# Kernel tuning notes

Measured on AMD Instinct MI355X. Metric: run time of the kernel, lower is better.

## Reference

```python
import jax, jax.numpy as jnp
import numpy as np

B, K = 4, 128
V_IN, V_OUT = 256, 256
E_IN, E_OUT = 512, 512
P_PE, T_PE = 200, 100
HEADS = 16  # c_atten_head


def _lin(key, din, dout):
    kw, kb = jax.random.split(key)
    W = jax.random.normal(kw, (din, dout), jnp.float32) / np.sqrt(din).astype(np.float32)
    b = jax.random.normal(kb, (dout,), jnp.float32) * 0.01
    return W, b


def setup_inputs() -> dict:
    key = jax.random.key(0)
    ks = jax.random.split(key, 14)
    v_f = jax.random.normal(ks[0], (B, K, V_IN), jnp.float32)
    e_f = jax.random.normal(ks[1], (B, K * K, E_IN), jnp.float32)
    p_pe = jax.random.normal(ks[2], (B, K, P_PE), jnp.float32)
    t_pe = jax.random.normal(ks[3], (B, T_PE), jnp.float32)
    e_agg_mask = (jax.random.uniform(ks[4], (B, K, K)) > 0.1).astype(jnp.float32)
    v_agg_mask = (jax.random.uniform(ks[5], (B, K)) > 0.1).astype(jnp.float32)
    W_vpe, b_vpe = _lin(ks[6], V_IN + P_PE + T_PE, V_IN)
    W_epe, b_epe = _lin(ks[7], E_IN + T_PE, E_IN)
    W_ev1, b_ev1 = _lin(ks[8], E_IN + 2 * V_IN, E_OUT)
    W_ev2, b_ev2 = _lin(ks[9], E_OUT, E_OUT)
    W_q, b_q = _lin(ks[10], V_IN, E_OUT)
    W_k, b_k = _lin(ks[11], V_IN, E_OUT)
    W_self, b_self = _lin(ks[12], V_IN, E_OUT)
    W_out, b_out = _lin(ks[13], 2 * E_OUT, V_OUT)
    return dict(v_f=v_f, e_f=e_f, p_pe=p_pe, t_pe=t_pe,
                e_agg_mask=e_agg_mask, v_agg_mask=v_agg_mask,
                W_vpe=W_vpe, b_vpe=b_vpe, W_epe=W_epe, b_epe=b_epe,
                W_ev1=W_ev1, b_ev1=b_ev1, W_ev2=W_ev2, b_ev2=b_ev2,
                W_q=W_q, b_q=b_q, W_k=W_k, b_k=b_k,
                W_self=W_self, b_self=b_self, W_out=W_out, b_out=b_out)


def reference(v_f, e_f, p_pe, t_pe, e_agg_mask, v_agg_mask,
              W_vpe, b_vpe, W_epe, b_epe, W_ev1, b_ev1, W_ev2, b_ev2,
              W_q, b_q, W_k, b_k, W_self, b_self, W_out, b_out):
    silu = jax.nn.silu
    # PE binding
    t_v = jnp.broadcast_to(t_pe[:, None, :], (B, K, T_PE))
    v = silu(jnp.concatenate([v_f, p_pe, t_v], -1) @ W_vpe + b_vpe)          # (B,K,V_IN)
    t_e = jnp.broadcast_to(t_pe[:, None, :], (B, K * K, T_PE))
    e = silu(jnp.concatenate([e_f, t_e], -1) @ W_epe + b_epe)                # (B,K*K,E_IN)
    # dense all-pairs node features -> edge values
    pair = jnp.concatenate([jnp.broadcast_to(v[:, :, None, :], (B, K, K, V_IN)),
                            jnp.broadcast_to(v[:, None, :, :], (B, K, K, V_IN))], -1)
    ev_in = jnp.concatenate([pair.reshape(B, K * K, 2 * V_IN), e], -1)
    e_value = silu(ev_in @ W_ev1 + b_ev1) @ W_ev2 + b_ev2                     # (B,K*K,E_OUT)
    agg_e = e_value.reshape(B, K, K, E_OUT)
    # elementwise-multiply / head-sum attention
    q = v @ W_q + b_q                                                         # (B,K,E_OUT)
    k = v @ W_k + b_k
    att = (q[:, :, None, :] * k[:, None, :, :]).reshape(B, K, K, E_OUT // HEADS, HEADS)
    att = att.sum(-1, keepdims=True) / np.float32(np.sqrt(HEADS * 3.0))       # (B,K,K,G,1)
    a = jax.nn.sigmoid(att) * e_agg_mask[..., None, None]
    a = a / (a.sum(2, keepdims=True) + 1e-6)
    a = jnp.broadcast_to(a, (B, K, K, E_OUT // HEADS, HEADS)).reshape(B, K, K, E_OUT)
    agg_v = (a * agg_e).sum(2)                                                # (B,K,E_OUT)
    v2 = agg_v + silu(v @ W_self + b_self)
    # masked max-pool over nodes
    pooled = (v2 - 1e9 * (1.0 - v_agg_mask)[..., None]).max(1, keepdims=True)
    pooled = jnp.broadcast_to(pooled, (B, K, E_OUT))
    v_out = silu(jnp.concatenate([v2, pooled], -1) @ W_out + b_out)           # (B,K,V_OUT)
    return v_out, e_value
```

## Files before the change

### kernel.cpp

```cpp
#include <hip/hip_runtime.h>

typedef unsigned short ushort_t;
typedef __attribute__((ext_vector_type(8))) short bf16x8;
typedef __attribute__((ext_vector_type(4))) float f32x4;

__device__ __forceinline__ ushort_t f2bf(float f) {
    union { float f; unsigned u; } v; v.f = f;
    unsigned r = v.u + 0x7FFFu + ((v.u >> 16) & 1u);
    return (ushort_t)(r >> 16);
}
__device__ __forceinline__ float siluf(float x) { return x / (1.f + __expf(-x)); }
__device__ __forceinline__ float sigm(float x)  { return 1.f / (1.f + __expf(-x)); }

__device__ __forceinline__ void gl2lds16(const void* g, void* l) {
    __builtin_amdgcn_global_load_lds(
        (__attribute__((address_space(1))) void*)(const_cast<void*>(g)),
        (__attribute__((address_space(3))) void*)(l), 16, 0, 0);
}

__global__ void k_pt(const float* W_epe, const float* W_ev1, const float* W_ev2,
                     const float* t_pe, const float* W_vpe, const float* b_vpe,
                     const float* b_epe,
                     ushort_t* WT_epe, ushort_t* WT_c, ushort_t* WT_ev2,
                     float* c_v, float* c_e) {
    int n = blockIdx.x, mat = blockIdx.y, t = threadIdx.x;
    if (mat == 3) {
        if (n < 4) {
            int b = n;
            for (int col = t; col < 512; col += 256) {
                float acc = b_epe[col];
                for (int u = 0; u < 100; ++u) acc += t_pe[b*100+u] * W_epe[(512+u)*512 + col];
                c_e[b*512 + col] = acc;
            }
            {
                float acc = b_vpe[t];
                for (int u = 0; u < 100; ++u) acc += t_pe[b*100+u] * W_vpe[(456+u)*256 + t];
                c_v[b*256 + t] = acc;
            }
        }
        return;
    }
    const float* src; ushort_t* dst;
    if (mat == 0)      { src = W_epe;            dst = WT_epe; }
    else if (mat == 1) { src = W_ev1 + 512*512;  dst = WT_c;   }
    else               { src = W_ev2;            dst = WT_ev2; }
    for (int k = t; k < 512; k += 256)
        dst[n*512 + k] = f2bf(src[k*512 + n]);
}

__global__ void k_node_v(const float* v_f, const float* p_pe, const float* W_vpe,
                         const float* c_v, float* v) {
    __shared__ float rv[4][256];
    __shared__ float rp[4][200];
    int r0 = blockIdx.x * 4, t = threadIdx.x;
    for (int rr = 0; rr < 4; ++rr) {
        rv[rr][t] = v_f[(r0+rr)*256 + t];
        if (t < 200) rp[rr][t] = p_pe[(r0+rr)*200 + t];
    }
    __syncthreads();
    int b = r0 >> 7;
    float acc[4];
    float cv = c_v[b*256 + t];
    for (int rr = 0; rr < 4; ++rr) acc[rr] = cv;
    for (int k = 0; k < 256; ++k) {
        float w = W_vpe[k*256 + t];
        #pragma unroll
        for (int rr = 0; rr < 4; ++rr) acc[rr] += rv[rr][k] * w;
    }
    for (int k = 0; k < 200; ++k) {
        float w = W_vpe[(256+k)*256 + t];
        #pragma unroll
        for (int rr = 0; rr < 4; ++rr) acc[rr] += rp[rr][k] * w;
    }
    for (int rr = 0; rr < 4; ++rr) v[(r0+rr)*256 + t] = siluf(acc[rr]);
}

__global__ void k_node_proj(const float* v,
                            const float* W_q, const float* b_q,
                            const float* W_k, const float* b_k,
                            const float* W_self, const float* b_self,
                            const float* W_ev1, const float* b_ev1,
                            float* q, float* kk, float* vs, float* P, float* Q) {
    __shared__ float rv[4][256];
    int r0 = blockIdx.x * 4, which = blockIdx.y, t = threadIdx.x;
    for (int rr = 0; rr < 4; ++rr) rv[rr][t] = v[(r0+rr)*256 + t];
    __syncthreads();
    const float* W; const float* bias = nullptr; float* out; bool do_silu = false;
    if (which == 0)      { W = W_q;    bias = b_q;    out = q;  }
    else if (which == 1) { W = W_k;    bias = b_k;    out = kk; }
    else if (which == 2) { W = W_self; bias = b_self; out = vs; do_silu = true; }
    else if (which == 3) { W = W_ev1;  bias = b_ev1;  out = P;  }
    else                 { W = W_ev1 + 256*512;       out = Q;  }
    float acc[4][2] = {};
    for (int k = 0; k < 256; ++k) {
        float w0 = W[k*512 + t];
        float w1 = W[k*512 + t + 256];
        #pragma unroll
        for (int rr = 0; rr < 4; ++rr) {
            acc[rr][0] += rv[rr][k] * w0;
            acc[rr][1] += rv[rr][k] * w1;
        }
    }
    float bb0 = bias ? bias[t] : 0.f;
    float bb1 = bias ? bias[t + 256] : 0.f;
    for (int rr = 0; rr < 4; ++rr) {
        float x0 = acc[rr][0] + bb0;
        float x1 = acc[rr][1] + bb1;
        if (do_silu) { x0 = siluf(x0); x1 = siluf(x1); }
        out[(r0+rr)*512 + t]       = x0;
        out[(r0+rr)*512 + t + 256] = x1;
    }
}

__global__ __launch_bounds__(256) void k_attw(const float* q, const float* kmat,
                                              const float* emask, float* anorm) {
    int bi = blockIdx.x; int b = bi >> 7, i = bi & 127;
    int t = threadIdx.x;
    __shared__ __align__(16) float qrow[512];
    __shared__ float s[128][33];
    __shared__ float invd[32];
    qrow[t]       = q[(size_t)bi*512 + t];
    qrow[t + 256] = q[(size_t)bi*512 + t + 256];
    __syncthreads();
    {
        int j = t >> 1, g0 = (t & 1) * 16;
        const float* kr = kmat + ((size_t)b*128 + j) * 512;
        float msk = emask[(size_t)b*16384 + i*128 + j];
        for (int gg = 0; gg < 16; ++gg) {
            int g = g0 + gg;
            const float4* k4 = (const float4*)(kr + g*16);
            const float4* q4 = (const float4*)(qrow + g*16);
            float acc = 0.f;
            #pragma unroll
            for (int c = 0; c < 4; ++c) {
                float4 kv = k4[c], qv = q4[c];
                acc += kv.x*qv.x + kv.y*qv.y + kv.z*qv.z + kv.w*qv.w;
            }
            s[j][g] = sigm(acc * 0.14433756729740645f) * msk;
        }
    }
    __syncthreads();
    if (t < 32) {
        float d = 1e-6f;
        for (int j = 0; j < 128; ++j) d += s[j][t];
        invd[t] = 1.f / d;
    }
    __syncthreads();
    float* dst = anorm + (size_t)bi * 4096;
    for (int idx = t; idx < 4096; idx += 256) {
        int j = idx >> 5, g = idx & 31;
        dst[idx] = s[j][g] * invd[g];
    }
}

template <int MODE>
__global__ __launch_bounds__(256) void k_gemm(const void* Aptr, const ushort_t* BT,
                                              const float* e0, const float* e1,
                                              const float* e2,
                                              ushort_t* out16, float* out32,
                                              float* v2out) {
    __shared__ __align__(16) ushort_t smem[32768];
    int lin = blockIdx.x;
    int xcd = lin & 7, idx = lin >> 3;
    int mt = xcd * 64 + (idx >> 2);
    int nt = idx & 3;
    int m0 = mt * 128, n0 = nt * 128;
    int t = threadIdx.x;
    int wv = t >> 6, lane = t & 63;
    int wm = (wv >> 1) * 64, wn = (wv & 1) * 64;
    int ml = lane & 15, quad = lane >> 4;
    f32x4 acc[4][4] = {};

    int brow = t >> 2, bseg = t & 3;
    const ushort_t* gB = BT + (size_t)(n0 + brow) * 512 + bseg * 8;
    const ushort_t* gA16 = (const ushort_t*)Aptr + (size_t)(m0 + brow) * 512 + bseg * 8;
    const float*    gA32 = (const float*)Aptr + (size_t)(m0 + (t >> 4)) * 512 + (t & 15) * 4;

    float4 f[8];
    int ahalf = (t >> 3) & 1;
    int acol  = (t & 7) * 4;

    auto issueB = [&](int it, int d) {
        int kk = it * 64;
        #pragma unroll
        for (int s = 0; s < 2; ++s)
            #pragma unroll
            for (int g = 0; g < 2; ++g)
                gl2lds16(gB + (size_t)g * 64 * 512 + kk + s * 32,
                         smem + 16384 + d * 8192 + s * 4096 + g * 2048 + wv * 512);
    };
    auto issueA16 = [&](int it, int d) {
        int kk = it * 64;
        #pragma unroll
        for (int s = 0; s < 2; ++s)
            #pragma unroll
            for (int g = 0; g < 2; ++g)
                gl2lds16(gA16 + (size_t)g * 64 * 512 + kk + s * 32,
                         smem + d * 8192 + s * 4096 + g * 2048 + wv * 512);
    };
    auto loadA32 = [&](int it) {
        int kk = it * 64;
        #pragma unroll
        for (int j = 0; j < 8; ++j)
            f[j] = *(const float4*)(gA32 + (size_t)(j * 16) * 512 + kk);
    };
    auto writeA32 = [&](int d) {
        #pragma unroll
        for (int j = 0; j < 8; ++j) {
            int row = (t >> 4) + j * 16;
            ushort_t* dst = smem + d * 8192 + ahalf * 4096 + row * 32 + acol;
            float4 v4 = f[j];
            *(ushort4*)dst = make_ushort4(f2bf(v4.x), f2bf(v4.y), f2bf(v4.z), f2bf(v4.w));
        }
    };
    auto compute = [&](int d) {
        #pragma unroll
        for (int s = 0; s < 2; ++s) {
            bf16x8 a[4], b[4];
            #pragma unroll
            for (int tm = 0; tm < 4; ++tm)
                a[tm] = *(const bf16x8*)(smem + d * 8192 + s * 4096 + (wm + tm*16 + ml) * 32 + quad * 8);
            #pragma unroll
            for (int tn = 0; tn < 4; ++tn)
                b[tn] = *(const bf16x8*)(smem + 16384 + d * 8192 + s * 4096 + (wn + tn*16 + ml) * 32 + quad * 8);
            #pragma unroll
            for (int tm = 0; tm < 4; ++tm)
                #pragma unroll
                for (int tn = 0; tn < 4; ++tn)
                    acc[tm][tn] = __builtin_amdgcn_mfma_f32_16x16x32_bf16(a[tm], b[tn], acc[tm][tn], 0, 0, 0);
        }
    };

    if (MODE == 0) { issueB(0, 0); loadA32(0); writeA32(0); }
    else           { issueB(0, 0); issueA16(0, 0); }

    for (int it = 0; it < 8; ++it) {
        __syncthreads();
        int nd = (it + 1) & 1;
        if (MODE == 0) {
            if (it < 7) { issueB(it + 1, nd); loadA32(it + 1); }
            compute(it & 1);
            if (it < 7) writeA32(nd);
        } else {
            if (it < 7) { issueB(it + 1, nd); issueA16(it + 1, nd); }
            compute(it & 1);
        }
    }

    int gn0 = n0 + wn + ml;
    if (MODE == 2) {
        __syncthreads();
        float* aw  = (float*)smem;
        float* red = aw + 4096;
        {
            const float4* src = (const float4*)(e1 + (size_t)mt * 4096);
            float4* dw = (float4*)aw;
            for (int i2 = t; i2 < 1024; i2 += 256) dw[i2] = src[i2];
        }
        __syncthreads();
        float bv[4];
        #pragma unroll
        for (int tn = 0; tn < 4; ++tn) bv[tn] = e0[gn0 + tn*16];
        float partial[4] = {0.f, 0.f, 0.f, 0.f};
        #pragma unroll
        for (int tm = 0; tm < 4; ++tm)
            #pragma unroll
            for (int tn = 0; tn < 4; ++tn)
                #pragma unroll
                for (int r = 0; r < 4; ++r) {
                    int j  = wm + tm*16 + quad*4 + r;
                    int gn = gn0 + tn*16;
                    float x = acc[tm][tn][r] + bv[tn];
                    out32[((size_t)m0 + j) * 512 + gn] = x;
                    partial[tn] += aw[j * 32 + (gn >> 4)] * x;
                }
        #pragma unroll
        for (int tn = 0; tn < 4; ++tn) {
            float p = partial[tn];
            p += __shfl_down(p, 32);
            p += __shfl_down(p, 16);
            if (quad == 0 && lane < 16) red[wv * 64 + tn * 16 + ml] = p;
        }
        __syncthreads();
        if (t < 128) {
            int c = t, half = c >> 6, cl = c & 63;
            float tot = red[half * 64 + cl] + red[(half + 2) * 64 + cl];
            size_t o = (size_t)mt * 512 + n0 + c;
            v2out[o] = tot + e2[o];
        }
    } else if (MODE == 1) {
        int bi = mt;
        int brow0 = (bi >> 7) << 7;
        float Pv[4];
        #pragma unroll
        for (int tn = 0; tn < 4; ++tn) Pv[tn] = e0[(size_t)bi * 512 + gn0 + tn*16];
        #pragma unroll
        for (int tm = 0; tm < 4; ++tm)
            #pragma unroll
            for (int tn = 0; tn < 4; ++tn)
                #pragma unroll
                for (int r = 0; r < 4; ++r) {
                    int j  = wm + tm*16 + quad*4 + r;
                    int gn = gn0 + tn*16;
                    float x = acc[tm][tn][r] + Pv[tn]
                            + e1[(size_t)(brow0 + j) * 512 + gn];
                    out16[((size_t)m0 + j) * 512 + gn] = f2bf(siluf(x));
                }
    } else {
        int b_ = mt >> 7;
        float cv[4];
        #pragma unroll
        for (int tn = 0; tn < 4; ++tn) cv[tn] = e0[b_ * 512 + gn0 + tn*16];
        #pragma unroll
        for (int tm = 0; tm < 4; ++tm)
            #pragma unroll
            for (int tn = 0; tn < 4; ++tn)
                #pragma unroll
                for (int r = 0; r < 4; ++r) {
                    int j  = wm + tm*16 + quad*4 + r;
                    int gn = gn0 + tn*16;
                    float x = acc[tm][tn][r] + cv[tn];
                    out16[((size_t)m0 + j) * 512 + gn] = f2bf(siluf(x));
                }
    }
}

__global__ __launch_bounds__(256) void k_out(const float* v2, const float* vmask,
                                             const float* W_out, const float* b_out,
                                             float* out) {
    __shared__ float pooled[512];
    __shared__ float rv[4][512];
    __shared__ float vm[128];
    int r0 = blockIdx.x * 4, t = threadIdx.x, b = r0 >> 7;
    if (t < 128) vm[t] = -1e9f * (1.f - vmask[b*128 + t]);
    for (int rr = 0; rr < 4; ++rr) {
        rv[rr][t]       = v2[(size_t)(r0+rr)*512 + t];
        rv[rr][t + 256] = v2[(size_t)(r0+rr)*512 + t + 256];
    }
    __syncthreads();
    for (int d = t; d < 512; d += 256) {
        float m = -1e30f;
        for (int i = 0; i < 128; ++i)
            m = fmaxf(m, v2[((size_t)(b*128 + i))*512 + d] + vm[i]);
        pooled[d] = m;
    }
    __syncthreads();
    float cp = b_out[t];
    for (int d = 0; d < 512; ++d) cp += pooled[d] * W_out[(512 + d)*256 + t];
    float acc[4];
    for (int rr = 0; rr < 4; ++rr) acc[rr] = cp;
    for (int k = 0; k < 512; ++k) {
        float w = W_out[k*256 + t];
        #pragma unroll
        for (int rr = 0; rr < 4; ++rr) acc[rr] += rv[rr][k] * w;
    }
    for (int rr = 0; rr < 4; ++rr) out[(r0+rr)*256 + t] = siluf(acc[rr]);
}

extern "C" void kernel_launch(void* const* d_in, const int* in_sizes, int n_in,
                              void* d_out, int out_size, void* d_ws, size_t ws_size,
                              hipStream_t stream) {
    const float* v_f    = (const float*)d_in[0];
    const float* e_f    = (const float*)d_in[1];
    const float* p_pe   = (const float*)d_in[2];
    const float* t_pe   = (const float*)d_in[3];
    const float* emask  = (const float*)d_in[4];
    const float* vmask  = (const float*)d_in[5];
    const float* W_vpe  = (const float*)d_in[6];
    const float* b_vpe  = (const float*)d_in[7];
    const float* W_epe  = (const float*)d_in[8];
    const float* b_epe  = (const float*)d_in[9];
    const float* W_ev1  = (const float*)d_in[10];
    const float* b_ev1  = (const float*)d_in[11];
    const float* W_ev2  = (const float*)d_in[12];
    const float* b_ev2  = (const float*)d_in[13];
    const float* W_q    = (const float*)d_in[14];
    const float* b_q    = (const float*)d_in[15];
    const float* W_k    = (const float*)d_in[16];
    const float* b_k    = (const float*)d_in[17];
    const float* W_self = (const float*)d_in[18];
    const float* b_self = (const float*)d_in[19];
    const float* W_out  = (const float*)d_in[20];
    const float* b_out  = (const float*)d_in[21];

    float* out_v = (float*)d_out;
    float* out_e = (float*)d_out + 131072;

    char* w = (char*)d_ws;
    ushort_t* WT_epe = (ushort_t*)w; w += 512*512*2;
    ushort_t* WT_c   = (ushort_t*)w; w += 512*512*2;
    ushort_t* WT_ev2 = (ushort_t*)w; w += 512*512*2;
    float* c_v   = (float*)w; w += 4*256*4;
    float* c_e   = (float*)w; w += 4*512*4;
    float* v     = (float*)w; w += 512*256*4;
    float* qbuf  = (float*)w; w += 512*512*4;
    float* kbuf  = (float*)w; w += 512*512*4;
    float* vsbuf = (float*)w; w += 512*512*4;
    float* Pbuf  = (float*)w; w += 512*512*4;
    float* Qbuf  = (float*)w; w += 512*512*4;
    float* v2buf = (float*)w; w += 512*512*4;
    float* anorm = (float*)w; w += (size_t)4*128*128*32*4;
    ushort_t* e16 = (ushort_t*)w; w += (size_t)65536*512*2;
    ushort_t* h16 = (ushort_t*)w; w += (size_t)65536*512*2;

    k_pt<<<dim3(512, 4), 256, 0, stream>>>(W_epe, W_ev1, W_ev2, t_pe, W_vpe, b_vpe, b_epe,
                                           WT_epe, WT_c, WT_ev2, c_v, c_e);
    k_node_v<<<128, 256, 0, stream>>>(v_f, p_pe, W_vpe, c_v, v);
    k_node_proj<<<dim3(128, 5), 256, 0, stream>>>(v, W_q, b_q, W_k, b_k, W_self, b_self,
                                                  W_ev1, b_ev1, qbuf, kbuf, vsbuf, Pbuf, Qbuf);
    k_attw<<<512, 256, 0, stream>>>(qbuf, kbuf, emask, anorm);
    k_gemm<0><<<2048, 256, 0, stream>>>(e_f, WT_epe, c_e, nullptr, nullptr, e16, nullptr, nullptr);
    k_gemm<1><<<2048, 256, 0, stream>>>(e16, WT_c, Pbuf, Qbuf, nullptr, h16, nullptr, nullptr);
    k_gemm<2><<<2048, 256, 0, stream>>>(h16, WT_ev2, b_ev2, anorm, vsbuf, nullptr, out_e, v2buf);
    k_out<<<128, 256, 0, stream>>>(v2buf, vmask, W_out, b_out, out_v);
}
```

Measured before the change: 646.7 us.

## Pre-tile bf16 operands in swizzled layout and deepen GEMM pipeline to four stages

A new kernel converts e_f to bf16 once, storing it in a tiled, XOR-swizzled layout. Weights and intermediate activations are written in the same layout, so every GEMM loads contiguous 16-byte chunks straight into LDS without bank conflicts. The GEMM main loop now uses a 4-slab ring with three k-chunks in flight, explicit vmcnt waits and raw barriers, plus setprio around the MFMA work. This removes the fp32 load-and-convert path from the first GEMM and the LDS bank conflicts. The cost is an extra conversion pass over e_f and a dependence on hand-written waitcnt counts for correctness.

```diff
diff --git a/kernel.cpp b/kernel.cpp
--- a/kernel.cpp
+++ b/kernel.cpp
@@ -16,6 +16,11 @@
     __builtin_amdgcn_global_load_lds(
         (__attribute__((address_space(1))) void*)(const_cast<void*>(g)),
         (__attribute__((address_space(3))) void*)(l), 16, 0, 0);
+}
+
+__device__ __forceinline__ size_t ts_idx(int mt, int j, int k) {
+    return (size_t)mt * 65536 + (size_t)((k >> 5) * 4096) + j * 32
+         + ((((k >> 3) & 3) ^ (j & 3)) * 8) + (k & 7);
 }
 
 __global__ void k_pt(const float* W_epe, const float* W_ev1, const float* W_ev2,
@@ -44,8 +49,19 @@
     if (mat == 0)      { src = W_epe;            dst = WT_epe; }
     else if (mat == 1) { src = W_ev1 + 512*512;  dst = WT_c;   }
     else               { src = W_ev2;            dst = WT_ev2; }
+    int nt_ = n >> 7, r = n & 127;
     for (int k = t; k < 512; k += 256)
-        dst[n*512 + k] = f2bf(src[k*512 + n]);
+        dst[ts_idx(nt_, r, k)] = f2bf(src[k*512 + n]);
+}
+
+__global__ __launch_bounds__(256) void k_cvt(const float* ef, ushort_t* dst) {
+    int idx = blockIdx.x * 256 + threadIdx.x;
+    int m = idx >> 6, k0 = (idx & 63) * 8;
+    const float4* s = (const float4*)(ef + (size_t)m * 512 + k0);
+    float4 a = s[0], b = s[1];
+    ushort_t* d = dst + ts_idx(m >> 7, m & 127, k0);
+    *(ushort4*)d       = make_ushort4(f2bf(a.x), f2bf(a.y), f2bf(a.z), f2bf(a.w));
+    *(ushort4*)(d + 4) = make_ushort4(f2bf(b.x), f2bf(b.y), f2bf(b.z), f2bf(b.w));
 }
 
 __global__ void k_node_v(const float* v_f, const float* p_pe, const float* W_vpe,
@@ -154,7 +170,7 @@
 }
 
 template <int MODE>
-__global__ __launch_bounds__(256) void k_gemm(const void* Aptr, const ushort_t* BT,
+__global__ __launch_bounds__(256) void k_gemm(const ushort_t* A, const ushort_t* BT,
                                               const float* e0, const float* e1,
                                               const float* e2,
                                               ushort_t* out16, float* out32,
@@ -164,87 +180,57 @@
     int xcd = lin & 7, idx = lin >> 3;
     int mt = xcd * 64 + (idx >> 2);
     int nt = idx & 3;
-    int m0 = mt * 128, n0 = nt * 128;
+    int n0 = nt * 128;
+    int m0 = mt * 128;
     int t = threadIdx.x;
     int wv = t >> 6, lane = t & 63;
     int wm = (wv >> 1) * 64, wn = (wv & 1) * 64;
     int ml = lane & 15, quad = lane >> 4;
+    int qs = (quad ^ (ml & 3)) * 8;
     f32x4 acc[4][4] = {};
 
-    int brow = t >> 2, bseg = t & 3;
-    const ushort_t* gB = BT + (size_t)(n0 + brow) * 512 + bseg * 8;
-    const ushort_t* gA16 = (const ushort_t*)Aptr + (size_t)(m0 + brow) * 512 + bseg * 8;
-    const float*    gA32 = (const float*)Aptr + (size_t)(m0 + (t >> 4)) * 512 + (t & 15) * 4;
-
-    float4 f[8];
-    int ahalf = (t >> 3) & 1;
-    int acol  = (t & 7) * 4;
-
-    auto issueB = [&](int it, int d) {
-        int kk = it * 64;
-        #pragma unroll
-        for (int s = 0; s < 2; ++s)
-            #pragma unroll
-            for (int g = 0; g < 2; ++g)
-                gl2lds16(gB + (size_t)g * 64 * 512 + kk + s * 32,
-                         smem + 16384 + d * 8192 + s * 4096 + g * 2048 + wv * 512);
+    const ushort_t* gA = A  + (size_t)mt * 65536 + wv * 512 + lane * 8;
+    const ushort_t* gB = BT + (size_t)nt * 65536 + wv * 512 + lane * 8;
+
+    auto issue = [&](int h) {
+        int slab = h & 3;
+        ushort_t* sA = smem + slab * 8192;
+        size_t off = (size_t)h * 4096;
+        #pragma unroll
+        for (int g = 0; g < 2; ++g) {
+            gl2lds16(gA + off + g * 2048, sA + (wv + g * 4) * 512);
+            gl2lds16(gB + off + g * 2048, sA + 4096 + (wv + g * 4) * 512);
+        }
     };
-    auto issueA16 = [&](int it, int d) {
-        int kk = it * 64;
-        #pragma unroll
-        for (int s = 0; s < 2; ++s)
-            #pragma unroll
-            for (int g = 0; g < 2; ++g)
-                gl2lds16(gA16 + (size_t)g * 64 * 512 + kk + s * 32,
-                         smem + d * 8192 + s * 4096 + g * 2048 + wv * 512);
-    };
-    auto loadA32 = [&](int it) {
-        int kk = it * 64;
-        #pragma unroll
-        for (int j = 0; j < 8; ++j)
-            f[j] = *(const float4*)(gA32 + (size_t)(j * 16) * 512 + kk);
-    };
-    auto writeA32 = [&](int d) {
-        #pragma unroll
-        for (int j = 0; j < 8; ++j) {
-            int row = (t >> 4) + j * 16;
-            ushort_t* dst = smem + d * 8192 + ahalf * 4096 + row * 32 + acol;
-            float4 v4 = f[j];
-            *(ushort4*)dst = make_ushort4(f2bf(v4.x), f2bf(v4.y), f2bf(v4.z), f2bf(v4.w));
-        }
-    };
-    auto compute = [&](int d) {
-        #pragma unroll
-        for (int s = 0; s < 2; ++s) {
-            bf16x8 a[4], b[4];
-            #pragma unroll
-            for (int tm = 0; tm < 4; ++tm)
-                a[tm] = *(const bf16x8*)(smem + d * 8192 + s * 4096 + (wm + tm*16 + ml) * 32 + quad * 8);
+    auto compute = [&](int h) {
+        int slab = h & 3;
+        const ushort_t* sA = smem + slab * 8192;
+        const ushort_t* sB = sA + 4096;
+        bf16x8 a[4], b[4];
+        #pragma unroll
+        for (int tm = 0; tm < 4; ++tm)
+            a[tm] = *(const bf16x8*)(sA + (wm + tm * 16 + ml) * 32 + qs);
+        #pragma unroll
+        for (int tn = 0; tn < 4; ++tn)
+            b[tn] = *(const bf16x8*)(sB + (wn + tn * 16 + ml) * 32 + qs);
+        #pragma unroll
+        for (int tm = 0; tm < 4; ++tm)
             #pragma unroll
             for (int tn = 0; tn < 4; ++tn)
-                b[tn] = *(const bf16x8*)(smem + 16384 + d * 8192 + s * 4096 + (wn + tn*16 + ml) * 32 + quad * 8);
-            #pragma unroll
-            for (int tm = 0; tm < 4; ++tm)
-                #pragma unroll
-                for (int tn = 0; tn < 4; ++tn)
-                    acc[tm][tn] = __builtin_amdgcn_mfma_f32_16x16x32_bf16(a[tm], b[tn], acc[tm][tn], 0, 0, 0);
-        }
+                acc[tm][tn] = __builtin_amdgcn_mfma_f32_16x16x32_bf16(a[tm], b[tn], acc[tm][tn], 0, 0, 0);
     };
 
-    if (MODE == 0) { issueB(0, 0); loadA32(0); writeA32(0); }
-    else           { issueB(0, 0); issueA16(0, 0); }
-
-    for (int it = 0; it < 8; ++it) {
-        __syncthreads();
-        int nd = (it + 1) & 1;
-        if (MODE == 0) {
-            if (it < 7) { issueB(it + 1, nd); loadA32(it + 1); }
-            compute(it & 1);
-            if (it < 7) writeA32(nd);
-        } else {
-            if (it < 7) { issueB(it + 1, nd); issueA16(it + 1, nd); }
-            compute(it & 1);
-        }
+    issue(0); issue(1); issue(2);
+    #pragma unroll
+    for (int h = 0; h < 16; ++h) {
+        if (h < 14)       asm volatile("s_waitcnt vmcnt(8) lgkmcnt(0)" ::: "memory");
+        else if (h == 14) asm volatile("s_waitcnt vmcnt(4) lgkmcnt(0)" ::: "memory");
+        else              asm volatile("s_waitcnt vmcnt(0) lgkmcnt(0)" ::: "memory");
+        __builtin_amdgcn_s_barrier();
+        if (h < 13) issue(h + 3);
+        __builtin_amdgcn_s_setprio(1);
+        compute(h);
+        __builtin_amdgcn_s_setprio(0);
     }
 
     int gn0 = n0 + wn + ml;
@@ -289,11 +275,10 @@
             v2out[o] = tot + e2[o];
         }
     } else if (MODE == 1) {
-        int bi = mt;
-        int brow0 = (bi >> 7) << 7;
+        int brow0 = (mt >> 7) << 7;
         float Pv[4];
         #pragma unroll
-        for (int tn = 0; tn < 4; ++tn) Pv[tn] = e0[(size_t)bi * 512 + gn0 + tn*16];
+        for (int tn = 0; tn < 4; ++tn) Pv[tn] = e0[(size_t)mt * 512 + gn0 + tn*16];
         #pragma unroll
         for (int tm = 0; tm < 4; ++tm)
             #pragma unroll
@@ -304,7 +289,7 @@
                     int gn = gn0 + tn*16;
                     float x = acc[tm][tn][r] + Pv[tn]
                             + e1[(size_t)(brow0 + j) * 512 + gn];
-                    out16[((size_t)m0 + j) * 512 + gn] = f2bf(siluf(x));
+                    out16[ts_idx(mt, j, gn)] = f2bf(siluf(x));
                 }
     } else {
         int b_ = mt >> 7;
@@ -320,7 +305,7 @@
                     int j  = wm + tm*16 + quad*4 + r;
                     int gn = gn0 + tn*16;
                     float x = acc[tm][tn][r] + cv[tn];
-                    out16[((size_t)m0 + j) * 512 + gn] = f2bf(siluf(x));
+                    out16[ts_idx(mt, j, gn)] = f2bf(siluf(x));
                 }
     }
 }
@@ -405,11 +390,12 @@
 
     k_pt<<<dim3(512, 4), 256, 0, stream>>>(W_epe, W_ev1, W_ev2, t_pe, W_vpe, b_vpe, b_epe,
                                            WT_epe, WT_c, WT_ev2, c_v, c_e);
+    k_cvt<<<16384, 256, 0, stream>>>(e_f, h16);
     k_node_v<<<128, 256, 0, stream>>>(v_f, p_pe, W_vpe, c_v, v);
     k_node_proj<<<dim3(128, 5), 256, 0, stream>>>(v, W_q, b_q, W_k, b_k, W_self, b_self,
                                                   W_ev1, b_ev1, qbuf, kbuf, vsbuf, Pbuf, Qbuf);
     k_attw<<<512, 256, 0, stream>>>(qbuf, kbuf, emask, anorm);
-    k_gemm<0><<<2048, 256, 0, stream>>>(e_f, WT_epe, c_e, nullptr, nullptr, e16, nullptr, nullptr);
+    k_gemm<0><<<2048, 256, 0, stream>>>(h16, WT_epe, c_e, nullptr, nullptr, e16, nullptr, nullptr);
     k_gemm<1><<<2048, 256, 0, stream>>>(e16, WT_c, Pbuf, Qbuf, nullptr, h16, nullptr, nullptr);
     k_gemm<2><<<2048, 256, 0, stream>>>(h16, WT_ev2, b_ev2, anorm, vsbuf, nullptr, out_e, v2buf);
     k_out<<<128, 256, 0, stream>>>(v2buf, vmask, W_out, b_out, out_v);
```

Result: faster. 598.1 us (-7.5%).
